# Optimization experiments

Measured on AMD Instinct MI355X. Metric: run time of the kernel, lower is better.

The kernel has to match this reference:

```python
import jax, jax.numpy as jnp
from jax import lax
import numpy as np

IN, HID, OUT = 28, 64, 10


def _lstm_layer(x_seq, W_ih, W_hh, b_ih, b_hh):
    # x_seq: [B, T, in]; PyTorch gate order: i, f, g, o (stacked along 4H)
    B = x_seq.shape[0]
    H = W_hh.shape[1]
    # Precompute input projection for all timesteps: [B, T, 4H]
    x_proj = jnp.einsum('bti,gi->btg', x_seq, W_ih) + b_ih + b_hh

    def step(carry, xt):
        h, c = carry
        gates = xt + h @ W_hh.T  # [B, 4H]
        i, f, g, o = jnp.split(gates, 4, axis=-1)
        i = jax.nn.sigmoid(i)
        f = jax.nn.sigmoid(f)
        g = jnp.tanh(g)
        o = jax.nn.sigmoid(o)
        c = f * c + i * g
        h = o * jnp.tanh(c)
        return (h, c), h

    h0 = jnp.zeros((B, H), x_seq.dtype)
    (_, _), hs = lax.scan(step, (h0, h0), jnp.swapaxes(x_proj, 0, 1))
    return jnp.swapaxes(hs, 0, 1)  # [B, T, H]


def setup_inputs() -> dict:
    key = jax.random.key(0)
    ks = jax.random.split(key, 12)
    s_in = 1.0 / np.sqrt(HID)
    u = lambda k, shape: jax.random.uniform(k, shape, jnp.float32, -s_in, s_in)
    return {
        'x': jax.random.normal(ks[0], (16384, 1, 28, 28), jnp.float32),
        'W_ih0': u(ks[1], (4 * HID, IN)),
        'W_hh0': u(ks[2], (4 * HID, HID)),
        'b_ih0': u(ks[3], (4 * HID,)),
        'b_hh0': u(ks[4], (4 * HID,)),
        'W_ih1': u(ks[5], (4 * HID, HID)),
        'W_hh1': u(ks[6], (4 * HID, HID)),
        'b_ih1': u(ks[7], (4 * HID,)),
        'b_hh1': u(ks[8], (4 * HID,)),
        'W_lin': u(ks[9], (OUT, HID)),
        'b_lin': u(ks[10], (OUT,)),
    }


def reference(x, W_ih0, W_hh0, b_ih0, b_hh0, W_ih1, W_hh1, b_ih1, b_hh1, W_lin, b_lin):
    # (N, C, H, W) -> (N, C*H, W): sequence of rows, feature = W = 28
    x = x.reshape(x.shape[0], -1, x.shape[-1])
    h1 = _lstm_layer(x, W_ih0, W_hh0, b_ih0, b_hh0)   # [B, T, 64]
    h2 = _lstm_layer(h1, W_ih1, W_hh1, b_ih1, b_hh1)  # [B, T, 64]
    last = h2[:, -1, :]
    return last @ W_lin.T + b_lin  # [B, 10]
```

## Files before the change

### kernel.cpp

```cpp
#include <hip/hip_runtime.h>


typedef _Float16 half8 __attribute__((ext_vector_type(8)));
typedef float floatx4 __attribute__((ext_vector_type(4)));

__device__ __forceinline__ float sigf(float v) {
    return __builtin_amdgcn_rcpf(1.0f + __expf(-v));
}
__device__ __forceinline__ float tanhf2(float v) {
    return 1.0f - 2.0f * __builtin_amdgcn_rcpf(__expf(2.0f * v) + 1.0f);
}

__launch_bounds__(512, 4)
__global__ void lstm_mfma(const float* __restrict__ x,
                          const float* __restrict__ Wih0, const float* __restrict__ Whh0,
                          const float* __restrict__ bih0, const float* __restrict__ bhh0,
                          const float* __restrict__ Wih1, const float* __restrict__ Whh1,
                          const float* __restrict__ bih1, const float* __restrict__ bhh1,
                          const float* __restrict__ Wlin, const float* __restrict__ blin,
                          float* __restrict__ out) {
    __shared__ __align__(16) _Float16 h0p[2][2048];
    __shared__ __align__(16) _Float16 h1p[2][2048];
    __shared__ __align__(16) _Float16 xb[2][1024];
    __shared__ float wlin_s[640];
    __shared__ float blin_s[10];

    const int lane = threadIdx.x;
    const int w    = threadIdx.y;
    const int tid  = w * 64 + lane;
    const int quad = lane >> 4;
    const int col  = lane & 15;

    half8 A0[2][3], A1[2][4];
    #pragma unroll
    for (int im = 0; im < 2; ++im) {
        int mt = 2 * w + im;
        int m  = mt * 16 + col;
        int u  = m >> 2, g = m & 3;
        int row = g * 64 + u;
        #pragma unroll
        for (int kt = 0; kt < 3; ++kt) {
            half8 r;
            #pragma unroll
            for (int j = 0; j < 8; ++j) {
                int k = kt * 32 + quad * 8 + j;
                float v;
                if (k < 28)       v = Wih0[row * 28 + k];
                else if (k == 28) v = bih0[row] + bhh0[row];
                else if (k < 32)  v = 0.f;
                else              v = Whh0[row * 64 + (k - 32)];
                r[j] = (_Float16)v;
            }
            A0[im][kt] = r;
        }
        #pragma unroll
        for (int kt = 0; kt < 4; ++kt) {
            half8 r;
            #pragma unroll
            for (int j = 0; j < 8; ++j) {
                int k = kt * 32 + quad * 8 + j;
                float v = (k < 64) ? Wih1[row * 64 + k] : Whh1[row * 64 + (k - 64)];
                r[j] = (_Float16)v;
            }
            A1[im][kt] = r;
        }
    }
    floatx4 bias1[2];
    #pragma unroll
    for (int im = 0; im < 2; ++im) {
        int u = (2 * w + im) * 4 + quad;
        #pragma unroll
        for (int r = 0; r < 4; ++r) bias1[im][r] = bih1[r * 64 + u] + bhh1[r * 64 + u];
    }

    int xrd[2], hrd[2][2], hwr[2][2];
    #pragma unroll
    for (int in = 0; in < 2; ++in) {
        xrd[in] = in * 512 + lane * 8;
        #pragma unroll
        for (int kt = 0; kt < 2; ++kt) hrd[kt][in] = (in * 2 + kt) * 512 + lane * 8;
        #pragma unroll
        for (int im = 0; im < 2; ++im) {
            int u = (2 * w + im) * 4 + quad;
            hwr[im][in] = (in * 2 + (u >> 5)) * 512 + (((u >> 3) & 3) * 16 + col) * 8 + (u & 7);
        }
    }

    const int xi = tid & 31;
    const bool xvalid = xi < 28;
    const float* xg[2];
    int xstg[2];
    #pragma unroll
    for (int s = 0; s < 2; ++s) {
        int b = (tid >> 5) + s * 16;
        xg[s]   = x + (blockIdx.x * 32 + b) * 784 + xi;
        xstg[s] = (b >> 4) * 512 + ((xi >> 3) * 16 + (b & 15)) * 8 + (xi & 7);
    }

    {
        int* z0 = (int*)&h0p[0][0];
        int* z1 = (int*)&h1p[0][0];
        #pragma unroll
        for (int i = tid; i < 1024; i += 512) { z0[i] = 0; z1[i] = 0; }
        #pragma unroll
        for (int s = 0; s < 2; ++s) {
            float xv = xvalid ? xg[s][0] : 0.f;
            xb[0][xstg[s]] = (xi == 28) ? (_Float16)1.0f : (_Float16)xv;
        }
    }
    __syncthreads();

    float c0[4] = {0.f, 0.f, 0.f, 0.f};
    float c1[4] = {0.f, 0.f, 0.f, 0.f};

    for (int t = 0; t < 28; ++t) {
        const int p = t & 1, q = p ^ 1;
        _Float16* h0r = h0p[p];
        _Float16* h0w = h0p[q];
        _Float16* h1r = h1p[p];
        _Float16* h1w = h1p[q];
        const _Float16* xr = xb[p];

        float xn[2] = {0.f, 0.f};
        if (t < 27) {
            #pragma unroll
            for (int s = 0; s < 2; ++s)
                if (xvalid) xn[s] = xg[s][(t + 1) * 28];
        }

        floatx4 acc0[2][2], acc1[2][2];
        #pragma unroll
        for (int im = 0; im < 2; ++im)
            #pragma unroll
            for (int in = 0; in < 2; ++in)
                acc0[im][in] = (floatx4){0.f, 0.f, 0.f, 0.f};

        #pragma unroll
        for (int in = 0; in < 2; ++in) {
            half8 bf = *(const half8*)&xr[xrd[in]];
            #pragma unroll
            for (int im = 0; im < 2; ++im)
                acc0[im][in] = __builtin_amdgcn_mfma_f32_16x16x32_f16(A0[im][0], bf, acc0[im][in], 0, 0, 0);
        }
        #pragma unroll
        for (int kt = 0; kt < 2; ++kt) {
            #pragma unroll
            for (int in = 0; in < 2; ++in) {
                half8 bf = *(const half8*)&h0r[hrd[kt][in]];
                #pragma unroll
                for (int im = 0; im < 2; ++im)
                    acc0[im][in] = __builtin_amdgcn_mfma_f32_16x16x32_f16(A0[im][kt + 1], bf, acc0[im][in], 0, 0, 0);
            }
        }

        #pragma unroll
        for (int im = 0; im < 2; ++im)
            #pragma unroll
            for (int in = 0; in < 2; ++in)
                acc1[im][in] = bias1[im];
        #pragma unroll
        for (int kt = 0; kt < 2; ++kt) {
            #pragma unroll
            for (int in = 0; in < 2; ++in) {
                half8 bf = *(const half8*)&h1r[hrd[kt][in]];
                #pragma unroll
                for (int im = 0; im < 2; ++im)
                    acc1[im][in] = __builtin_amdgcn_mfma_f32_16x16x32_f16(A1[im][kt + 2], bf, acc1[im][in], 0, 0, 0);
            }
        }

        #pragma unroll
        for (int im = 0; im < 2; ++im) {
            #pragma unroll
            for (int in = 0; in < 2; ++in) {
                floatx4 a = acc0[im][in];
                float ig = sigf(a[0]), fg = sigf(a[1]), gg = tanhf2(a[2]), og = sigf(a[3]);
                float c = fg * c0[im * 2 + in] + ig * gg;
                c0[im * 2 + in] = c;
                h0w[hwr[im][in]] = (_Float16)(og * tanhf2(c));
            }
        }
        __syncthreads();

        #pragma unroll
        for (int kt = 0; kt < 2; ++kt) {
            #pragma unroll
            for (int in = 0; in < 2; ++in) {
                half8 bf = *(const half8*)&h0w[hrd[kt][in]];
                #pragma unroll
                for (int im = 0; im < 2; ++im)
                    acc1[im][in] = __builtin_amdgcn_mfma_f32_16x16x32_f16(A1[im][kt], bf, acc1[im][in], 0, 0, 0);
            }
        }

        #pragma unroll
        for (int im = 0; im < 2; ++im) {
            #pragma unroll
            for (int in = 0; in < 2; ++in) {
                floatx4 a = acc1[im][in];
                float ig = sigf(a[0]), fg = sigf(a[1]), gg = tanhf2(a[2]), og = sigf(a[3]);
                float c = fg * c1[im * 2 + in] + ig * gg;
                c1[im * 2 + in] = c;
                h1w[hwr[im][in]] = (_Float16)(og * tanhf2(c));
            }
        }
        if (t < 27) {
            #pragma unroll
            for (int s = 0; s < 2; ++s)
                xb[q][xstg[s]] = (xi == 28) ? (_Float16)1.0f : (_Float16)xn[s];
        }
        __syncthreads();
    }

    #pragma unroll
    for (int i = tid; i < 640; i += 512) wlin_s[i] = Wlin[i];
    if (tid < 10) blin_s[tid] = blin[tid];
    __syncthreads();
    if (tid < 320) {
        int b = tid / 10, o = tid - b * 10;
        float a = blin_s[o];
        #pragma unroll 8
        for (int u = 0; u < 64; ++u) {
            float hv = (float)h1p[0][((b >> 4) * 2 + (u >> 5)) * 512 + (((u >> 3) & 3) * 16 + (b & 15)) * 8 + (u & 7)];
            a += wlin_s[o * 64 + u] * hv;
        }
        out[(blockIdx.x * 32 + b) * 10 + o] = a;
    }
}

extern "C" void kernel_launch(void* const* d_in, const int* in_sizes, int n_in,
                              void* d_out, int out_size, void* d_ws, size_t ws_size,
                              hipStream_t stream) {
    const float* x    = (const float*)d_in[0];
    const float* Wih0 = (const float*)d_in[1];
    const float* Whh0 = (const float*)d_in[2];
    const float* bih0 = (const float*)d_in[3];
    const float* bhh0 = (const float*)d_in[4];
    const float* Wih1 = (const float*)d_in[5];
    const float* Whh1 = (const float*)d_in[6];
    const float* bih1 = (const float*)d_in[7];
    const float* bhh1 = (const float*)d_in[8];
    const float* Wlin = (const float*)d_in[9];
    const float* blin = (const float*)d_in[10];
    float* out = (float*)d_out;

    lstm_mfma<<<512, dim3(64, 8), 0, stream>>>(x, Wih0, Whh0, bih0, bhh0,
                                               Wih1, Whh1, bih1, bhh1, Wlin, blin, out);
}
```

Baseline: 202.0 us.

## Skew layer-1 by one timestep to drop one barrier per step

Restructures the time loop as a wavefront: each iteration computes layer 0 at step p+1 and layer 1 at step p, both reading the same h0 buffer. This removes the mid-step __syncthreads, leaving one barrier per iteration, and shares the loaded h0 fragments between both layers' MFMAs. It adds one extra iteration for prologue and epilogue and reshuffles the double-buffer parity for h0, h1 and x, which raises the risk of indexing mistakes.

```diff
diff --git a/kernel.cpp b/kernel.cpp
--- a/kernel.cpp
+++ b/kernel.cpp
@@ -98,8 +98,8 @@
     }
 
     {
-        int* z0 = (int*)&h0p[0][0];
-        int* z1 = (int*)&h1p[0][0];
+        int* z0 = (int*)&h0p[1][0];
+        int* z1 = (int*)&h1p[1][0];
         #pragma unroll
         for (int i = tid; i < 1024; i += 512) { z0[i] = 0; z1[i] = 0; }
         #pragma unroll
@@ -113,101 +113,101 @@
     float c0[4] = {0.f, 0.f, 0.f, 0.f};
     float c1[4] = {0.f, 0.f, 0.f, 0.f};
 
-    for (int t = 0; t < 28; ++t) {
-        const int p = t & 1, q = p ^ 1;
-        _Float16* h0r = h0p[p];
-        _Float16* h0w = h0p[q];
-        _Float16* h1r = h1p[p];
-        _Float16* h1w = h1p[q];
-        const _Float16* xr = xb[p];
+    for (int p = -1; p <= 27; ++p) {
+        const int pr  = p & 1;
+        const int pr1 = pr ^ 1;
+        const bool doL0 = (p < 27);
+        const bool doL1 = (p >= 0);
 
         float xn[2] = {0.f, 0.f};
-        if (t < 27) {
+        if (p <= 25) {
             #pragma unroll
             for (int s = 0; s < 2; ++s)
-                if (xvalid) xn[s] = xg[s][(t + 1) * 28];
-        }
-
-        floatx4 acc0[2][2], acc1[2][2];
-        #pragma unroll
-        for (int im = 0; im < 2; ++im)
+                if (xvalid) xn[s] = xg[s][(p + 2) * 28];
+        }
+
+        half8 bh0[2][2];
+        #pragma unroll
+        for (int kt = 0; kt < 2; ++kt)
             #pragma unroll
             for (int in = 0; in < 2; ++in)
-                acc0[im][in] = (floatx4){0.f, 0.f, 0.f, 0.f};
-
-        #pragma unroll
-        for (int in = 0; in < 2; ++in) {
-            half8 bf = *(const half8*)&xr[xrd[in]];
+                bh0[kt][in] = *(const half8*)&h0p[pr][hrd[kt][in]];
+
+        if (doL0) {
+            floatx4 acc0[2][2];
             #pragma unroll
             for (int im = 0; im < 2; ++im)
-                acc0[im][in] = __builtin_amdgcn_mfma_f32_16x16x32_f16(A0[im][0], bf, acc0[im][in], 0, 0, 0);
-        }
-        #pragma unroll
-        for (int kt = 0; kt < 2; ++kt) {
+                #pragma unroll
+                for (int in = 0; in < 2; ++in)
+                    acc0[im][in] = (floatx4){0.f, 0.f, 0.f, 0.f};
             #pragma unroll
             for (int in = 0; in < 2; ++in) {
-                half8 bf = *(const half8*)&h0r[hrd[kt][in]];
+                half8 bf = *(const half8*)&xb[pr1][xrd[in]];
                 #pragma unroll
                 for (int im = 0; im < 2; ++im)
-                    acc0[im][in] = __builtin_amdgcn_mfma_f32_16x16x32_f16(A0[im][kt + 1], bf, acc0[im][in], 0, 0, 0);
-            }
-        }
-
-        #pragma unroll
-        for (int im = 0; im < 2; ++im)
-            #pragma unroll
-            for (int in = 0; in < 2; ++in)
-                acc1[im][in] = bias1[im];
-        #pragma unroll
-        for (int kt = 0; kt < 2; ++kt) {
-            #pragma unroll
-            for (int in = 0; in < 2; ++in) {
-                half8 bf = *(const half8*)&h1r[hrd[kt][in]];
-                #pragma unroll
-                for (int im = 0; im < 2; ++im)
-                    acc1[im][in] = __builtin_amdgcn_mfma_f32_16x16x32_f16(A1[im][kt + 2], bf, acc1[im][in], 0, 0, 0);
-            }
-        }
-
-        #pragma unroll
-        for (int im = 0; im < 2; ++im) {
-            #pragma unroll
-            for (int in = 0; in < 2; ++in) {
-                floatx4 a = acc0[im][in];
-                float ig = sigf(a[0]), fg = sigf(a[1]), gg = tanhf2(a[2]), og = sigf(a[3]);
-                float c = fg * c0[im * 2 + in] + ig * gg;
-                c0[im * 2 + in] = c;
-                h0w[hwr[im][in]] = (_Float16)(og * tanhf2(c));
-            }
-        }
-        __syncthreads();
-
-        #pragma unroll
-        for (int kt = 0; kt < 2; ++kt) {
-            #pragma unroll
-            for (int in = 0; in < 2; ++in) {
-                half8 bf = *(const half8*)&h0w[hrd[kt][in]];
-                #pragma unroll
-                for (int im = 0; im < 2; ++im)
-                    acc1[im][in] = __builtin_amdgcn_mfma_f32_16x16x32_f16(A1[im][kt], bf, acc1[im][in], 0, 0, 0);
-            }
-        }
-
-        #pragma unroll
-        for (int im = 0; im < 2; ++im) {
-            #pragma unroll
-            for (int in = 0; in < 2; ++in) {
-                floatx4 a = acc1[im][in];
-                float ig = sigf(a[0]), fg = sigf(a[1]), gg = tanhf2(a[2]), og = sigf(a[3]);
-                float c = fg * c1[im * 2 + in] + ig * gg;
-                c1[im * 2 + in] = c;
-                h1w[hwr[im][in]] = (_Float16)(og * tanhf2(c));
-            }
-        }
-        if (t < 27) {
+                    acc0[im][in] = __builtin_amdgcn_mfma_f32_16x16x32_f16(A0[im][0], bf, acc0[im][in], 0, 0, 0);
+            }
+            #pragma unroll
+            for (int kt = 0; kt < 2; ++kt)
+                #pragma unroll
+                for (int in = 0; in < 2; ++in)
+                    #pragma unroll
+                    for (int im = 0; im < 2; ++im)
+                        acc0[im][in] = __builtin_amdgcn_mfma_f32_16x16x32_f16(A0[im][kt + 1], bh0[kt][in], acc0[im][in], 0, 0, 0);
+            #pragma unroll
+            for (int im = 0; im < 2; ++im) {
+                #pragma unroll
+                for (int in = 0; in < 2; ++in) {
+                    floatx4 a = acc0[im][in];
+                    float ig = sigf(a[0]), fg = sigf(a[1]), gg = tanhf2(a[2]), og = sigf(a[3]);
+                    float c = fg * c0[im * 2 + in] + ig * gg;
+                    c0[im * 2 + in] = c;
+                    h0p[pr1][hwr[im][in]] = (_Float16)(og * tanhf2(c));
+                }
+            }
+        }
+
+        if (doL1) {
+            floatx4 acc1[2][2];
+            #pragma unroll
+            for (int im = 0; im < 2; ++im)
+                #pragma unroll
+                for (int in = 0; in < 2; ++in)
+                    acc1[im][in] = bias1[im];
+            #pragma unroll
+            for (int kt = 0; kt < 2; ++kt)
+                #pragma unroll
+                for (int in = 0; in < 2; ++in)
+                    #pragma unroll
+                    for (int im = 0; im < 2; ++im)
+                        acc1[im][in] = __builtin_amdgcn_mfma_f32_16x16x32_f16(A1[im][kt], bh0[kt][in], acc1[im][in], 0, 0, 0);
+            #pragma unroll
+            for (int kt = 0; kt < 2; ++kt) {
+                #pragma unroll
+                for (int in = 0; in < 2; ++in) {
+                    half8 bf = *(const half8*)&h1p[pr1][hrd[kt][in]];
+                    #pragma unroll
+                    for (int im = 0; im < 2; ++im)
+                        acc1[im][in] = __builtin_amdgcn_mfma_f32_16x16x32_f16(A1[im][kt + 2], bf, acc1[im][in], 0, 0, 0);
+                }
+            }
+            #pragma unroll
+            for (int im = 0; im < 2; ++im) {
+                #pragma unroll
+                for (int in = 0; in < 2; ++in) {
+                    floatx4 a = acc1[im][in];
+                    float ig = sigf(a[0]), fg = sigf(a[1]), gg = tanhf2(a[2]), og = sigf(a[3]);
+                    float c = fg * c1[im * 2 + in] + ig * gg;
+                    c1[im * 2 + in] = c;
+                    h1p[pr][hwr[im][in]] = (_Float16)(og * tanhf2(c));
+                }
+            }
+        }
+
+        if (p <= 25) {
             #pragma unroll
             for (int s = 0; s < 2; ++s)
-                xb[q][xstg[s]] = (xi == 28) ? (_Float16)1.0f : (_Float16)xn[s];
+                xb[pr][xstg[s]] = (xi == 28) ? (_Float16)1.0f : (_Float16)xn[s];
         }
         __syncthreads();
     }
@@ -221,7 +221,7 @@
         float a = blin_s[o];
         #pragma unroll 8
         for (int u = 0; u < 64; ++u) {
-            float hv = (float)h1p[0][((b >> 4) * 2 + (u >> 5)) * 512 + (((u >> 3) & 3) * 16 + (b & 15)) * 8 + (u & 7)];
+            float hv = (float)h1p[1][((b >> 4) * 2 + (u >> 5)) * 512 + (((u >> 3) & 3) * 16 + (b & 15)) * 8 + (u & 7)];
             a += wlin_s[o * 64 + u] * hv;
         }
         out[(blockIdx.x * 32 + b) * 10 + o] = a;
```

Measured after the change: 197.9 us. -2.1%, faster.
